# Optimization experiments

Measured on AMD Instinct MI355X. Metric: run time of the kernel, lower is better.

The kernel has to match this reference:

```python
import jax, jax.numpy as jnp
import numpy as np

C = 512
RED = 8
CK = C // RED  # 64


def setup_inputs() -> dict:
    key = jax.random.key(0)
    ks = jax.random.split(key, 7)
    B, L = 16, 2048
    scale = 1.0 / np.sqrt(C)
    x = jax.random.normal(ks[0], (B, C, L), dtype=jnp.float32)
    Wq = jax.random.normal(ks[1], (CK, C), dtype=jnp.float32) * scale
    bq = jnp.zeros((CK,), dtype=jnp.float32)
    Wk = jax.random.normal(ks[2], (CK, C), dtype=jnp.float32) * scale
    bk = jnp.zeros((CK,), dtype=jnp.float32)
    Wv = jax.random.normal(ks[3], (C, C), dtype=jnp.float32) * scale
    bv = jnp.zeros((C,), dtype=jnp.float32)
    gamma = jnp.zeros((1,), dtype=jnp.float32)
    return {"x": x, "Wq": Wq, "bq": bq, "Wk": Wk, "bk": bk,
            "Wv": Wv, "bv": bv, "gamma": gamma}


def reference(x, Wq, bq, Wk, bk, Wv, bv, gamma):
    # 1x1 conv == per-position linear over channel dim
    q = jnp.einsum('kc,bcl->bkl', Wq, x) + bq[None, :, None]   # (B, CK, L)
    k = jnp.einsum('kc,bcl->bkl', Wk, x) + bk[None, :, None]   # (B, CK, L)
    v = jnp.einsum('vc,bcl->bvl', Wv, x) + bv[None, :, None]   # (B, C, L)
    # attention[b, i, j] = sum_k q[b,k,i] * k[b,k,j]
    scores = jnp.einsum('bki,bkj->bij', q, k)                  # (B, L, L)
    attn = jax.nn.softmax(scores, axis=-1)
    # out[b,c,i] = sum_j v[b,c,j] * attn[b,i,j]
    out = jnp.einsum('bcj,bij->bci', v, attn)                  # (B, C, L)
    return gamma[0] * out + x
```

## Files before the change

kernel.cpp:

```cpp
#include <hip/hip_runtime.h>
#include <math.h>

static constexpr int B_  = 16;
static constexpr int C_  = 512;
static constexpr int L_  = 2048;

typedef __attribute__((ext_vector_type(8))) short bf16x8;
typedef __attribute__((ext_vector_type(4))) float f32x4;

__device__ __forceinline__ unsigned short f2bf(float f) {
    unsigned int u = __float_as_uint(f);
    unsigned int r = (u + 0x7FFFu + ((u >> 16) & 1u)) >> 16;
    return (unsigned short)r;
}

__device__ __forceinline__ void async_copy16(const void* g, void* l) {
    __builtin_amdgcn_global_load_lds(
        (const __attribute__((address_space(1))) unsigned int*)g,
        (__attribute__((address_space(3))) unsigned int*)l, 16, 0, 0);
}

__global__ __launch_bounds__(256)
void cast_w_kernel(const float* __restrict__ Wq, const float* __restrict__ Wk,
                   const float* __restrict__ Wv, unsigned short* __restrict__ Wb)
{
    const int idx = (blockIdx.x * 256 + threadIdx.x) * 8;
    const int m = idx >> 9;
    const int c = idx & 511;
    const float* src = (m < 64) ? (Wq + (size_t)m * 512)
                     : (m < 128) ? (Wk + (size_t)(m - 64) * 512)
                                 : (Wv + (size_t)(m - 128) * 512);
    float4 a = *(const float4*)(src + c);
    float4 d = *(const float4*)(src + c + 4);
    union { unsigned short h[8]; uint4 v; } o;
    o.h[0]=f2bf(a.x); o.h[1]=f2bf(a.y); o.h[2]=f2bf(a.z); o.h[3]=f2bf(a.w);
    o.h[4]=f2bf(d.x); o.h[5]=f2bf(d.y); o.h[6]=f2bf(d.z); o.h[7]=f2bf(d.w);
    *(uint4*)(Wb + idx) = o.v;
}

__global__ __launch_bounds__(256)
void cast_x_kernel(const float* __restrict__ x, unsigned short* __restrict__ xt)
{
    __shared__ float T[64][65];
    const int t  = threadIdx.x;
    const int l0 = blockIdx.x * 64;
    const int c0 = blockIdx.y * 64;
    const int b  = blockIdx.z;

    {
        const int cr = t >> 2;
        const int lc = (t & 3) * 16;
        const float* src = x + ((size_t)b * 512 + c0 + cr) * 2048 + l0 + lc;
        #pragma unroll
        for (int e4 = 0; e4 < 4; ++e4) {
            float4 f = *(const float4*)(src + e4 * 4);
            T[lc + e4*4 + 0][cr] = f.x;
            T[lc + e4*4 + 1][cr] = f.y;
            T[lc + e4*4 + 2][cr] = f.z;
            T[lc + e4*4 + 3][cr] = f.w;
        }
    }
    __syncthreads();
    {
        const int lr = t >> 2;
        const int cc = (t & 3) * 16;
        union { unsigned short h[16]; uint4 v[2]; } o;
        #pragma unroll
        for (int e = 0; e < 16; ++e) o.h[e] = f2bf(T[lr][cc + e]);
        unsigned short* dst = xt + ((size_t)b * 2048 + l0 + lr) * 512 + c0 + cc;
        *(uint4*)(dst + 0) = o.v[0];
        *(uint4*)(dst + 8) = o.v[1];
    }
}

__global__ __launch_bounds__(256)
void proj_mfma_kernel(const unsigned short* __restrict__ xt,
                      const unsigned short* __restrict__ Wb,
                      const float* __restrict__ bq, const float* __restrict__ bk,
                      const float* __restrict__ bv,
                      unsigned short* __restrict__ qt, unsigned short* __restrict__ kt,
                      unsigned short* __restrict__ v)
{
    __shared__ unsigned short As[128 * 64];
    __shared__ unsigned short Bs[128 * 64];

    const int t    = threadIdx.x;
    const int l0   = blockIdx.x * 128;
    const int c0t  = blockIdx.y * 128;
    const int b    = blockIdx.z;
    const int w    = t >> 6;
    const int lane = t & 63;
    const int quad = lane >> 4;
    const int n16  = lane & 15;
    const int mq   = (w & 1) * 64;
    const int nq   = (w >> 1) * 64;
    const int sr   = lane >> 3;
    const int sc   = (lane & 7) * 8;

    f32x4 acc[4][4];
    #pragma unroll
    for (int i = 0; i < 4; ++i)
        #pragma unroll
        for (int j = 0; j < 4; ++j) acc[i][j] = (f32x4){0.f,0.f,0.f,0.f};

    for (int kt_ = 0; kt_ < 512; kt_ += 64) {
        #pragma unroll
        for (int p = 0; p < 4; ++p) {
            const int rbase = w * 32 + p * 8;
            async_copy16(xt + ((size_t)(b * 2048 + l0 + rbase + sr)) * 512 + kt_ + sc,
                         &As[rbase * 64]);
            async_copy16(Wb + ((size_t)(c0t + rbase + sr)) * 512 + kt_ + sc,
                         &Bs[rbase * 64]);
        }
        __syncthreads();

        #pragma unroll
        for (int ks = 0; ks < 2; ++ks) {
            bf16x8 a[4], bb[4];
            #pragma unroll
            for (int mt = 0; mt < 4; ++mt)
                a[mt] = *(const bf16x8*)&As[(mq + mt*16 + n16) * 64 + ks*32 + quad*8];
            #pragma unroll
            for (int nt = 0; nt < 4; ++nt)
                bb[nt] = *(const bf16x8*)&Bs[(nq + nt*16 + n16) * 64 + ks*32 + quad*8];
            #pragma unroll
            for (int mt = 0; mt < 4; ++mt)
                #pragma unroll
                for (int nt = 0; nt < 4; ++nt)
                    acc[mt][nt] = __builtin_amdgcn_mfma_f32_16x16x32_bf16(a[mt], bb[nt], acc[mt][nt], 0, 0, 0);
        }
        __syncthreads();
    }

    #pragma unroll
    for (int nt = 0; nt < 4; ++nt) {
        const int crow = c0t + nq + nt*16 + n16;
        const float bias = (crow < 64) ? bq[crow] : (crow < 128) ? bk[crow - 64] : bv[crow - 128];
        #pragma unroll
        for (int mt = 0; mt < 4; ++mt) {
            const int lb = l0 + mq + mt*16 + quad*4;
            if (crow < 64) {
                #pragma unroll
                for (int r = 0; r < 4; ++r)
                    qt[((size_t)b * 2048 + lb + r) * 64 + crow] = f2bf(acc[mt][nt][r] + bias);
            } else if (crow < 128) {
                #pragma unroll
                for (int r = 0; r < 4; ++r)
                    kt[((size_t)b * 2048 + lb + r) * 64 + crow - 64] = f2bf(acc[mt][nt][r] + bias);
            } else {
                ushort4 o;
                o.x = f2bf(acc[mt][nt][0] + bias);
                o.y = f2bf(acc[mt][nt][1] + bias);
                o.z = f2bf(acc[mt][nt][2] + bias);
                o.w = f2bf(acc[mt][nt][3] + bias);
                *(ushort4*)(v + ((size_t)b * 512 + crow - 128) * 2048 + lb) = o;
            }
        }
    }
}

__global__ __launch_bounds__(256, 2)
void attn_kernel(const unsigned short* __restrict__ qt,
                 const unsigned short* __restrict__ kt,
                 const unsigned short* __restrict__ vg,
                 const float* __restrict__ x,
                 const float* __restrict__ gamma,
                 float* __restrict__ out)
{
    __shared__ unsigned short Ks[2][64 * 64];
    __shared__ unsigned short Ps[2][64][72];
    __shared__ float l_sh[64];
    __shared__ float Osc[4][16 * 20];

    const int t    = threadIdx.x;
    const int b    = blockIdx.y;
    const int i0b  = blockIdx.x * 64;
    const int w    = t >> 6;
    const int lane = t & 63;
    const int quad = lane >> 4;
    const int n16  = lane & 15;
    const int sr   = lane >> 3;
    const int sc   = (lane & 7) * 8;

    bf16x8 Qf[2];
    {
        const unsigned short* qp = qt + ((size_t)b * 2048 + i0b + w*16 + n16) * 64 + quad * 8;
        Qf[0] = *(const bf16x8*)(qp);
        Qf[1] = *(const bf16x8*)(qp + 32);
    }

    const unsigned short* kbase = kt + (size_t)b * 2048 * 64;
    const unsigned short* vbase = vg + ((size_t)b * 512 + w * 128 + n16) * 2048;

    #pragma unroll
    for (int p = 0; p < 2; ++p) {
        const int rbase = w * 16 + p * 8;
        async_copy16(kbase + (size_t)(rbase + sr) * 64 + sc, &Ks[0][rbase * 64]);
    }

    float l_part[4] = {0.f, 0.f, 0.f, 0.f};
    f32x4 O[8][4];
    #pragma unroll
    for (int ct = 0; ct < 8; ++ct)
        #pragma unroll
        for (int qb = 0; qb < 4; ++qb) O[ct][qb] = (f32x4){0.f,0.f,0.f,0.f};

    __syncthreads();

    for (int t32 = 0; t32 < 32; ++t32) {
        const int j0 = t32 * 64;
        const int cb = t32 & 1;
        const int nb = cb ^ 1;

        {
            const int j0n = (j0 + 64) & 2047;
            #pragma unroll
            for (int p = 0; p < 2; ++p) {
                const int rbase = w * 16 + p * 8;
                async_copy16(kbase + (size_t)(j0n + rbase + sr) * 64 + sc, &Ks[nb][rbase * 64]);
            }
        }

        bf16x8 VfA[4];
        #pragma unroll
        for (int i = 0; i < 4; ++i)
            VfA[i] = *(const bf16x8*)(vbase + (size_t)i * 16 * 2048 + j0 + quad * 8);

        f32x4 s[4];
        #pragma unroll
        for (int jb = 0; jb < 4; ++jb) {
            const unsigned short* kp = &Ks[cb][(jb*16 + n16) * 64 + quad * 8];
            bf16x8 kf0 = *(const bf16x8*)(kp);
            bf16x8 kf1 = *(const bf16x8*)(kp + 32);
            s[jb] = (f32x4){0.f,0.f,0.f,0.f};
            s[jb] = __builtin_amdgcn_mfma_f32_16x16x32_bf16(Qf[0], kf0, s[jb], 0, 0, 0);
            s[jb] = __builtin_amdgcn_mfma_f32_16x16x32_bf16(Qf[1], kf1, s[jb], 0, 0, 0);
        }

        #pragma unroll
        for (int jb = 0; jb < 4; ++jb) {
            #pragma unroll
            for (int r = 0; r < 4; ++r) {
                const float pv = __expf(s[jb][r] - 80.0f);
                l_part[r] += pv;
                Ps[cb][w*16 + quad*4 + r][jb*16 + n16] = f2bf(pv);
            }
        }

        __syncthreads();

        bf16x8 Pf[4];
        #pragma unroll
        for (int g = 0; g < 4; ++g) {
            const int ks  = g >> 1;
            const int ct2 = g & 1;
            bf16x8 VfB[4];
            if (g < 3) {
                const int ksn = (g + 1) >> 1, ct2n = (g + 1) & 1;
                #pragma unroll
                for (int i = 0; i < 4; ++i)
                    VfB[i] = *(const bf16x8*)(vbase + (size_t)(ct2n*4 + i) * 16 * 2048 + j0 + ksn*32 + quad*8);
            }
            if (ct2 == 0) {
                #pragma unroll
                for (int qb = 0; qb < 4; ++qb)
                    Pf[qb] = *(const bf16x8*)&Ps[cb][qb*16 + n16][ks*32 + quad*8];
            }
            #pragma unroll
            for (int i = 0; i < 4; ++i)
                #pragma unroll
                for (int qb = 0; qb < 4; ++qb)
                    O[ct2*4 + i][qb] = __builtin_amdgcn_mfma_f32_16x16x32_bf16(VfA[i], Pf[qb], O[ct2*4 + i][qb], 0, 0, 0);
            #pragma unroll
            for (int i = 0; i < 4; ++i) VfA[i] = VfB[i];
        }
    }

    #pragma unroll
    for (int r = 0; r < 4; ++r) {
        float sm = l_part[r];
        sm += __shfl_xor(sm, 1);
        sm += __shfl_xor(sm, 2);
        sm += __shfl_xor(sm, 4);
        sm += __shfl_xor(sm, 8);
        if (n16 == 0) l_sh[w*16 + quad*4 + r] = sm;
    }
    __syncthreads();

    {
        const float g = gamma[0];
        float linv[4];
        #pragma unroll
        for (int qb = 0; qb < 4; ++qb) linv[qb] = 1.0f / l_sh[qb*16 + n16];

        #pragma unroll
        for (int ct = 0; ct < 8; ++ct) {
            #pragma unroll
            for (int qb = 0; qb < 4; ++qb) {
                #pragma unroll
                for (int r = 0; r < 4; ++r)
                    Osc[w][(quad*4 + r) * 20 + n16] = O[ct][qb][r] * linv[qb];
                __builtin_amdgcn_wave_barrier();
                float4 ov = *(const float4*)&Osc[w][n16 * 20 + quad*4];
                __builtin_amdgcn_wave_barrier();
                const int c = w*128 + ct*16 + n16;
                const int i = i0b + qb*16 + quad*4;
                const size_t off = ((size_t)b * 512 + c) * 2048 + i;
                float4 xv = *(const float4*)(x + off);
                float4 o;
                o.x = fmaf(g, ov.x, xv.x);
                o.y = fmaf(g, ov.y, xv.y);
                o.z = fmaf(g, ov.z, xv.z);
                o.w = fmaf(g, ov.w, xv.w);
                *(float4*)(out + off) = o;
            }
        }
    }
}

extern "C" void kernel_launch(void* const* d_in, const int* in_sizes, int n_in,
                              void* d_out, int out_size, void* d_ws, size_t ws_size,
                              hipStream_t stream)
{
    const float* x     = (const float*)d_in[0];
    const float* Wq    = (const float*)d_in[1];
    const float* bq    = (const float*)d_in[2];
    const float* Wk    = (const float*)d_in[3];
    const float* bk    = (const float*)d_in[4];
    const float* Wv    = (const float*)d_in[5];
    const float* bv    = (const float*)d_in[6];
    const float* gamma = (const float*)d_in[7];
    float* out = (float*)d_out;

    unsigned short* ws = (unsigned short*)d_ws;
    unsigned short* xt = ws;
    unsigned short* v  = xt + (size_t)B_ * L_ * C_;
    unsigned short* qt = v  + (size_t)B_ * C_ * L_;
    unsigned short* kt = qt + (size_t)B_ * L_ * 64;
    unsigned short* Wb = kt + (size_t)B_ * L_ * 64;

    cast_w_kernel<<<160, 256, 0, stream>>>(Wq, Wk, Wv, Wb);
    dim3 gx(L_ / 64, C_ / 64, B_);
    cast_x_kernel<<<gx, 256, 0, stream>>>(x, xt);
    dim3 gp(L_ / 128, 640 / 128, B_);
    proj_mfma_kernel<<<gp, 256, 0, stream>>>(xt, Wb, bq, bk, bv, qt, kt, v);
    dim3 ga(L_ / 64, B_);
    attn_kernel<<<ga, 256, 0, stream>>>(qt, kt, v, x, gamma, out);
}
```

Baseline: 335.2 us.

## Stage V through double-buffered LDS via async copies and keep K in registers

The attention loop now prefetches the next V tile into a double-buffered shared-memory region with global_load_lds, instead of each wave reading V fragments straight from global memory. K fragments are loaded directly into registers one step ahead, replacing the K shared-memory staging. The key tile shrinks from 64 to 32 columns, so there are twice as many iterations and barriers. Shared memory is merged into one 76 KB buffer, with the epilogue scratch aliased onto the P buffer. The aim is to hide V load latency behind the MFMA work, at the cost of more shared memory per block and more frequent synchronisation.

After: 311.3 us. -7.1%, faster.

```diff
diff --git a/kernel.cpp b/kernel.cpp
--- a/kernel.cpp
+++ b/kernel.cpp
@@ -167,10 +167,11 @@
                  const float* __restrict__ gamma,
                  float* __restrict__ out)
 {
-    __shared__ unsigned short Ks[2][64 * 64];
-    __shared__ unsigned short Ps[2][64][72];
-    __shared__ float l_sh[64];
-    __shared__ float Osc[4][16 * 20];
+    __shared__ __align__(16) char smem[76032];
+    unsigned short* Vs   = (unsigned short*)smem;
+    unsigned short* Ps   = (unsigned short*)(smem + 65536);
+    float*          l_sh = (float*)(smem + 75776);
+    float*          Osc  = (float*)(smem + 65536);
 
     const int t    = threadIdx.x;
     const int b    = blockIdx.y;
@@ -179,8 +180,6 @@
     const int lane = t & 63;
     const int quad = lane >> 4;
     const int n16  = lane & 15;
-    const int sr   = lane >> 3;
-    const int sc   = (lane & 7) * 8;
 
     bf16x8 Qf[2];
     {
@@ -190,12 +189,23 @@
     }
 
     const unsigned short* kbase = kt + (size_t)b * 2048 * 64;
-    const unsigned short* vbase = vg + ((size_t)b * 512 + w * 128 + n16) * 2048;
-
-    #pragma unroll
-    for (int p = 0; p < 2; ++p) {
-        const int rbase = w * 16 + p * 8;
-        async_copy16(kbase + (size_t)(rbase + sr) * 64 + sc, &Ks[0][rbase * 64]);
+    const unsigned short* vbase = vg + (size_t)b * 512 * 2048;
+
+    const int vrow_in  = lane >> 2;
+    const int vcol_in  = (lane & 3) * 8;
+
+    bf16x8 Kc[2][2], Kn[2][2];
+    #pragma unroll
+    for (int jb = 0; jb < 2; ++jb)
+        #pragma unroll
+        for (int h = 0; h < 2; ++h)
+            Kc[jb][h] = *(const bf16x8*)(kbase + (size_t)(jb*16 + n16) * 64 + h*32 + quad*8);
+
+    #pragma unroll
+    for (int p = 0; p < 8; ++p) {
+        const int row = w*128 + p*16 + vrow_in;
+        async_copy16(vbase + (size_t)row * 2048 + vcol_in,
+                     Vs + (size_t)(w*128 + p*16) * 32 + (lane * 8));
     }
 
     float l_part[4] = {0.f, 0.f, 0.f, 0.f};
@@ -207,73 +217,63 @@
 
     __syncthreads();
 
-    for (int t32 = 0; t32 < 32; ++t32) {
-        const int j0 = t32 * 64;
-        const int cb = t32 & 1;
+    for (int it = 0; it < 64; ++it) {
+        const int j0 = it * 32;
+        const int cb = it & 1;
         const int nb = cb ^ 1;
-
-        {
-            const int j0n = (j0 + 64) & 2047;
-            #pragma unroll
-            for (int p = 0; p < 2; ++p) {
-                const int rbase = w * 16 + p * 8;
-                async_copy16(kbase + (size_t)(j0n + rbase + sr) * 64 + sc, &Ks[nb][rbase * 64]);
-            }
-        }
-
-        bf16x8 VfA[4];
-        #pragma unroll
-        for (int i = 0; i < 4; ++i)
-            VfA[i] = *(const bf16x8*)(vbase + (size_t)i * 16 * 2048 + j0 + quad * 8);
-
-        f32x4 s[4];
-        #pragma unroll
-        for (int jb = 0; jb < 4; ++jb) {
-            const unsigned short* kp = &Ks[cb][(jb*16 + n16) * 64 + quad * 8];
-            bf16x8 kf0 = *(const bf16x8*)(kp);
-            bf16x8 kf1 = *(const bf16x8*)(kp + 32);
+        const int j0n = (j0 + 32) & 2047;
+
+        f32x4 s[2];
+        #pragma unroll
+        for (int jb = 0; jb < 2; ++jb) {
             s[jb] = (f32x4){0.f,0.f,0.f,0.f};
-            s[jb] = __builtin_amdgcn_mfma_f32_16x16x32_bf16(Qf[0], kf0, s[jb], 0, 0, 0);
-            s[jb] = __builtin_amdgcn_mfma_f32_16x16x32_bf16(Qf[1], kf1, s[jb], 0, 0, 0);
-        }
-
-        #pragma unroll
-        for (int jb = 0; jb < 4; ++jb) {
+            s[jb] = __builtin_amdgcn_mfma_f32_16x16x32_bf16(Qf[0], Kc[jb][0], s[jb], 0, 0, 0);
+            s[jb] = __builtin_amdgcn_mfma_f32_16x16x32_bf16(Qf[1], Kc[jb][1], s[jb], 0, 0, 0);
+        }
+
+        #pragma unroll
+        for (int jb = 0; jb < 2; ++jb) {
             #pragma unroll
             for (int r = 0; r < 4; ++r) {
                 const float pv = __expf(s[jb][r] - 80.0f);
                 l_part[r] += pv;
-                Ps[cb][w*16 + quad*4 + r][jb*16 + n16] = f2bf(pv);
+                Ps[(size_t)cb * (64*40) + (w*16 + quad*4 + r) * 40 + jb*16 + n16] = f2bf(pv);
             }
         }
 
         __syncthreads();
 
-        bf16x8 Pf[4];
-        #pragma unroll
-        for (int g = 0; g < 4; ++g) {
-            const int ks  = g >> 1;
-            const int ct2 = g & 1;
-            bf16x8 VfB[4];
-            if (g < 3) {
-                const int ksn = (g + 1) >> 1, ct2n = (g + 1) & 1;
-                #pragma unroll
-                for (int i = 0; i < 4; ++i)
-                    VfB[i] = *(const bf16x8*)(vbase + (size_t)(ct2n*4 + i) * 16 * 2048 + j0 + ksn*32 + quad*8);
+        #pragma unroll
+        for (int p = 0; p < 8; ++p) {
+            const int row = w*128 + p*16 + vrow_in;
+            async_copy16(vbase + (size_t)row * 2048 + j0n + vcol_in,
+                         Vs + (size_t)nb * (512*32) + (size_t)(w*128 + p*16) * 32 + (lane * 8));
+        }
+        #pragma unroll
+        for (int jb = 0; jb < 2; ++jb)
+            #pragma unroll
+            for (int h = 0; h < 2; ++h)
+                Kn[jb][h] = *(const bf16x8*)(kbase + (size_t)(j0n + jb*16 + n16) * 64 + h*32 + quad*8);
+
+        {
+            bf16x8 Pf[4];
+            #pragma unroll
+            for (int qb = 0; qb < 4; ++qb)
+                Pf[qb] = *(const bf16x8*)&Ps[(size_t)cb * (64*40) + (qb*16 + n16) * 40 + quad*8];
+            #pragma unroll
+            for (int ct = 0; ct < 8; ++ct) {
+                bf16x8 Vf = *(const bf16x8*)&Vs[(size_t)cb * (512*32) + (w*128 + ct*16 + n16) * 32 + quad*8];
+                #pragma unroll
+                for (int qb = 0; qb < 4; ++qb)
+                    O[ct][qb] = __builtin_amdgcn_mfma_f32_16x16x32_bf16(Vf, Pf[qb], O[ct][qb], 0, 0, 0);
             }
-            if (ct2 == 0) {
-                #pragma unroll
-                for (int qb = 0; qb < 4; ++qb)
-                    Pf[qb] = *(const bf16x8*)&Ps[cb][qb*16 + n16][ks*32 + quad*8];
-            }
-            #pragma unroll
-            for (int i = 0; i < 4; ++i)
-                #pragma unroll
-                for (int qb = 0; qb < 4; ++qb)
-                    O[ct2*4 + i][qb] = __builtin_amdgcn_mfma_f32_16x16x32_bf16(VfA[i], Pf[qb], O[ct2*4 + i][qb], 0, 0, 0);
-            #pragma unroll
-            for (int i = 0; i < 4; ++i) VfA[i] = VfB[i];
-        }
+        }
+
+        #pragma unroll
+        for (int jb = 0; jb < 2; ++jb)
+            #pragma unroll
+            for (int h = 0; h < 2; ++h)
+                Kc[jb][h] = Kn[jb][h];
     }
 
     #pragma unroll
@@ -292,6 +292,7 @@
         float linv[4];
         #pragma unroll
         for (int qb = 0; qb < 4; ++qb) linv[qb] = 1.0f / l_sh[qb*16 + n16];
+        float* Ow = Osc + w * 320;
 
         #pragma unroll
         for (int ct = 0; ct < 8; ++ct) {
@@ -299,9 +300,9 @@
             for (int qb = 0; qb < 4; ++qb) {
                 #pragma unroll
                 for (int r = 0; r < 4; ++r)
-                    Osc[w][(quad*4 + r) * 20 + n16] = O[ct][qb][r] * linv[qb];
+                    Ow[(quad*4 + r) * 20 + n16] = O[ct][qb][r] * linv[qb];
                 __builtin_amdgcn_wave_barrier();
-                float4 ov = *(const float4*)&Osc[w][n16 * 20 + quad*4];
+                float4 ov = *(const float4*)&Ow[n16 * 20 + quad*4];
                 __builtin_amdgcn_wave_barrier();
                 const int c = w*128 + ct*16 + n16;
                 const int i = i0b + qb*16 + quad*4;
```
